# Performance work log

Hardware: AMD Instinct MI355X
Metric: run time of the kernel (lower is better)

## Reference

```python
import jax, jax.numpy as jnp
import numpy as np

B, C, H, WID = 32, 64, 128, 128
K = 5            # co-occurrence bins (co_shape)
WH = 3           # spatial filter height/width (w_shape = (1,3,3), depth 1)
ACT_LO, ACT_HI = 0.0, 1.0  # actBounds


def setup_inputs() -> dict:
    key = jax.random.key(0)
    k1, k2, k3 = jax.random.split(key, 3)
    input_tensor = jax.random.uniform(k1, (B, C, H, WID), dtype=jnp.float32)
    # learned params: L ~ N(0, 0.1) of shape (k,k); W ~ N(0,0.1) of shape (d,h,w)
    L = 0.1 * jax.random.normal(k2, (K, K), dtype=jnp.float32)
    W = 0.1 * jax.random.normal(k3, (1, WH, WH), dtype=jnp.float32)
    return {"input_tensor": input_tensor, "W": W, "L": L}


def _quantize(x, k):
    # map activation in [ACT_LO, ACT_HI] to bin index in [0, k-1]
    b = jnp.floor((x - ACT_LO) / (ACT_HI - ACT_LO) * k)
    return jnp.clip(b, 0, k - 1).astype(jnp.int32)


def reference(input_tensor, W, L):
    """Co-occurrence layer:
    out[p] = sum_{q in 3x3 nbhd(p)} W[q-p] * L[bin(x[q]), bin(x[p])] * x[q]
    Out-of-bounds neighbors contribute 0 (zero pad => x[q]=0 kills the term),
    matching the precomputed neighbor_lookup_table boundary handling.
    """
    k = L.shape[0]
    pad = WH // 2
    bins = _quantize(input_tensor, k)                      # (B,C,H,W) int32
    xp = jnp.pad(input_tensor, ((0, 0), (0, 0), (pad, pad), (pad, pad)))
    bp = jnp.pad(bins, ((0, 0), (0, 0), (pad, pad), (pad, pad)))
    h, w = input_tensor.shape[2], input_tensor.shape[3]
    out = jnp.zeros_like(input_tensor)
    for dh in range(WH):                                   # tiny fixed 3x3 loop
        for dw in range(WH):
            xn = xp[:, :, dh:dh + h, dw:dw + w]            # shifted neighbor values
            bn = bp[:, :, dh:dh + h, dw:dw + w]            # shifted neighbor bins
            out = out + W[0, dh, dw] * L[bn, bins] * xn    # gather L + weighted acc
    return out
```

## Files before the change

kernel.cpp:

```cpp
#include <hip/hip_runtime.h>


namespace {
constexpr int H  = 128;
constexpr int WD = 128;
constexpr int PLANES = 32 * 64;
constexpr int PX = 8;
constexpr int THREADS = 256;
}

__global__ __launch_bounds__(THREADS, 2) void col_kernel(
    const float* __restrict__ x, const float* __restrict__ Wf,
    const float* __restrict__ Lf, float* __restrict__ out)
{
    __shared__ float WL[9 * 25];
    const int t = threadIdx.x;
    if (t < 225) WL[t] = Wf[t / 25] * Lf[t % 25];
    __syncthreads();

    const int col0 = (t & 15) * PX;
    const int r0   = (t >> 4) * 8;

    const float* xp = x + (size_t)blockIdx.x * (H * WD);
    float* opb      = out + (size_t)blockIdx.x * (H * WD);
    const char* wlb = (const char*)WL;

    float win[4][PX + 2];
    int   bq[4][PX + 2];
    float n0[PX + 2], n1[PX + 2];

#define LOAD_ROW(DST, RR) {                                               \
    const int _rr = (RR);                                                 \
    if (_rr >= 0 && _rr < H) {                                            \
        const float* _rp = xp + _rr * WD + col0;                          \
        const float4 _c0 = *(const float4*)_rp;          \
        const float4 _c1 = *(const float4*)(_rp + 4);                     \
        DST[0] = (col0 > 0) ? _rp[-1] : 0.f;                              \
        DST[1] = _c0.x; DST[2] = _c0.y; DST[3] = _c0.z; DST[4] = _c0.w;   \
        DST[5] = _c1.x; DST[6] = _c1.y; DST[7] = _c1.z; DST[8] = _c1.w;   \
        DST[9] = (col0 < WD - PX) ? _rp[PX] : 0.f;                        \
    } else {                                                              \
        _Pragma("unroll")                                                 \
        for (int _j = 0; _j < PX + 2; ++_j) DST[_j] = 0.f;                \
    } }

#define QUANT_ROW(S) {                                                    \
    _Pragma("unroll")                                                     \
    for (int _j = 0; _j < PX + 2; ++_j) {                                 \
        int _b = (int)(win[S][_j] * 5.0f);        \
        _b = (_b > 4) ? 4 : _b;                                           \
        bq[S][_j] = _b * 20;                                              \
    } }

#define RETIRE(S, SRC) {                                                  \
    _Pragma("unroll")                                                     \
    for (int _j = 0; _j < PX + 2; ++_j) win[S][_j] = SRC[_j];             \
    QUANT_ROW(S) }

#define TERMS(QS, DR, BP, ACC) {                                          \
    _Pragma("unroll")                                                     \
    for (int _dw = 0; _dw < 3; ++_dw) {                                   \
        float _lw[PX];                                                    \
        _Pragma("unroll")                                                 \
        for (int _i = 0; _i < PX; ++_i)                                   \
            _lw[_i] = *(const float*)(wlb +                               \
                (bq[QS][_i + _dw] + BP[_i] + ((DR) * 3 + _dw) * 100));    \
        _Pragma("unroll")                                                 \
        for (int _i = 0; _i < PX; ++_i)                                   \
            ACC[_i] = fmaf(_lw[_i], win[QS][_i + _dw], ACC[_i]);          \
    } }

#define COMPUTE2(PA, PB, PC, PD, R) {                                     \
    int bp4a[PX], bp4b[PX];                                               \
    _Pragma("unroll")                                                     \
    for (int _i = 0; _i < PX; ++_i) {                                     \
        bp4a[_i] = (bq[PB][_i + 1] * 52429) >> 18;       \
        bp4b[_i] = (bq[PC][_i + 1] * 52429) >> 18;                        \
    }                                                                     \
    float acca[PX], accb[PX];                                             \
    _Pragma("unroll")                                                     \
    for (int _i = 0; _i < PX; ++_i) { acca[_i] = 0.f; accb[_i] = 0.f; }   \
    TERMS(PA, 0, bp4a, acca)                                              \
    TERMS(PB, 0, bp4b, accb)                                              \
    TERMS(PB, 1, bp4a, acca)                                              \
    TERMS(PC, 1, bp4b, accb)                                              \
    TERMS(PC, 2, bp4a, acca)                                              \
    TERMS(PD, 2, bp4b, accb)                                              \
    float* _op = opb + (R) * WD + col0;                                   \
    *(float4*)_op            = make_float4(acca[0], acca[1], acca[2], acca[3]); \
    *(float4*)(_op + 4)      = make_float4(acca[4], acca[5], acca[6], acca[7]); \
    *(float4*)(_op + WD)     = make_float4(accb[0], accb[1], accb[2], accb[3]); \
    *(float4*)(_op + WD + 4) = make_float4(accb[4], accb[5], accb[6], accb[7]); \
    }

    LOAD_ROW(win[0], r0 - 1) QUANT_ROW(0)
    LOAD_ROW(win[1], r0 + 0) QUANT_ROW(1)
    LOAD_ROW(win[2], r0 + 1) QUANT_ROW(2)
    LOAD_ROW(win[3], r0 + 2) QUANT_ROW(3)

    LOAD_ROW(n0, r0 + 3)
    LOAD_ROW(n1, r0 + 4)
    COMPUTE2(0, 1, 2, 3, r0)
    RETIRE(0, n0) RETIRE(1, n1)

    LOAD_ROW(n0, r0 + 5)
    LOAD_ROW(n1, r0 + 6)
    COMPUTE2(2, 3, 0, 1, r0 + 2)
    RETIRE(2, n0) RETIRE(3, n1)

    LOAD_ROW(n0, r0 + 7)
    LOAD_ROW(n1, r0 + 8)
    COMPUTE2(0, 1, 2, 3, r0 + 4)
    RETIRE(0, n0) RETIRE(1, n1)

    COMPUTE2(2, 3, 0, 1, r0 + 6)

#undef LOAD_ROW
#undef QUANT_ROW
#undef RETIRE
#undef TERMS
#undef COMPUTE2
}

extern "C" void kernel_launch(void* const* d_in, const int* in_sizes, int n_in,
                              void* d_out, int out_size, void* d_ws, size_t ws_size,
                              hipStream_t stream) {
    const float* x  = (const float*)d_in[0];
    const float* Wf = (const float*)d_in[1];
    const float* Lf = (const float*)d_in[2];
    float* out = (float*)d_out;

    col_kernel<<<dim3(PLANES), dim3(THREADS), 0, stream>>>(x, Wf, Lf, out);
}
```

Baseline: 252.2 us.

## Shrink register footprint with byte-packed bins and 3-row rolling window

Replaces the 4-row window plus two prefetch rows with a 3-row rolling window that computes one output row at a time, and packs the quantized bin offsets into bytes inside three ints per row. Launch bounds are raised from 2 to 5 blocks per CU to take advantage of the lower register use. The aim is higher occupancy to hide LDS-gather and global-load latency. In exchange there is less ILP per thread, less prefetch distance for the next row's loads, and extra shift/mask work to unpack each bin.

```diff
diff --git a/kernel.cpp b/kernel.cpp
--- a/kernel.cpp
+++ b/kernel.cpp
@@ -9,7 +9,7 @@
 constexpr int THREADS = 256;
 }
 
-__global__ __launch_bounds__(THREADS, 2) void col_kernel(
+__global__ __launch_bounds__(THREADS, 5) void col_kernel(
     const float* __restrict__ x, const float* __restrict__ Wf,
     const float* __restrict__ Lf, float* __restrict__ out)
 {
@@ -25,101 +25,87 @@
     float* opb      = out + (size_t)blockIdx.x * (H * WD);
     const char* wlb = (const char*)WL;
 
-    float win[4][PX + 2];
-    int   bq[4][PX + 2];
-    float n0[PX + 2], n1[PX + 2];
+    float win[3][PX + 2];
+    int   pk[3][3];
 
-#define LOAD_ROW(DST, RR) {                                               \
+#define LOAD_ROW(S, RR) {                                                 \
     const int _rr = (RR);                                                 \
     if (_rr >= 0 && _rr < H) {                                            \
         const float* _rp = xp + _rr * WD + col0;                          \
         const float4 _c0 = *(const float4*)_rp;          \
         const float4 _c1 = *(const float4*)(_rp + 4);                     \
-        DST[0] = (col0 > 0) ? _rp[-1] : 0.f;                              \
-        DST[1] = _c0.x; DST[2] = _c0.y; DST[3] = _c0.z; DST[4] = _c0.w;   \
-        DST[5] = _c1.x; DST[6] = _c1.y; DST[7] = _c1.z; DST[8] = _c1.w;   \
-        DST[9] = (col0 < WD - PX) ? _rp[PX] : 0.f;                        \
+        win[S][0] = (col0 > 0) ? _rp[-1] : 0.f;                           \
+        win[S][1] = _c0.x; win[S][2] = _c0.y;                             \
+        win[S][3] = _c0.z; win[S][4] = _c0.w;                             \
+        win[S][5] = _c1.x; win[S][6] = _c1.y;                             \
+        win[S][7] = _c1.z; win[S][8] = _c1.w;                             \
+        win[S][9] = (col0 < WD - PX) ? _rp[PX] : 0.f;                     \
     } else {                                                              \
         _Pragma("unroll")                                                 \
-        for (int _j = 0; _j < PX + 2; ++_j) DST[_j] = 0.f;                \
+        for (int _j = 0; _j < PX + 2; ++_j) win[S][_j] = 0.f;             \
     } }
 
-#define QUANT_ROW(S) {                                                    \
+#define QPACK(S) {                                                        \
+    int _b[PX + 2];                                                       \
     _Pragma("unroll")                                                     \
     for (int _j = 0; _j < PX + 2; ++_j) {                                 \
-        int _b = (int)(win[S][_j] * 5.0f);        \
-        _b = (_b > 4) ? 4 : _b;                                           \
-        bq[S][_j] = _b * 20;                                              \
-    } }
+        int _v = (int)(win[S][_j] * 5.0f);        \
+        _v = (_v > 4) ? 4 : _v;                                           \
+        _b[_j] = _v * 20;                                                 \
+    }                                                                     \
+    pk[S][0] = _b[0] | (_b[1] << 8) | (_b[2] << 16) | (_b[3] << 24);      \
+    pk[S][1] = _b[4] | (_b[5] << 8) | (_b[6] << 16) | (_b[7] << 24);      \
+    pk[S][2] = _b[8] | (_b[9] << 8); }
 
-#define RETIRE(S, SRC) {                                                  \
-    _Pragma("unroll")                                                     \
-    for (int _j = 0; _j < PX + 2; ++_j) win[S][_j] = SRC[_j];             \
-    QUANT_ROW(S) }
+#define BF(S, J) ((pk[S][(J) >> 2] >> (8 * ((J) & 3))) & 0xff)
 
-#define TERMS(QS, DR, BP, ACC) {                                          \
+#define TERMS(QS, DR) {                                                   \
     _Pragma("unroll")                                                     \
     for (int _dw = 0; _dw < 3; ++_dw) {                                   \
         float _lw[PX];                                                    \
         _Pragma("unroll")                                                 \
         for (int _i = 0; _i < PX; ++_i)                                   \
             _lw[_i] = *(const float*)(wlb +                               \
-                (bq[QS][_i + _dw] + BP[_i] + ((DR) * 3 + _dw) * 100));    \
+                (BF(QS, _i + _dw) + bp4[_i] + ((DR) * 3 + _dw) * 100));   \
         _Pragma("unroll")                                                 \
         for (int _i = 0; _i < PX; ++_i)                                   \
-            ACC[_i] = fmaf(_lw[_i], win[QS][_i + _dw], ACC[_i]);          \
+            acc[_i] = fmaf(_lw[_i], win[QS][_i + _dw], acc[_i]);          \
     } }
 
-#define COMPUTE2(PA, PB, PC, PD, R) {                                     \
-    int bp4a[PX], bp4b[PX];                                               \
+#define COMPUTE(A, B, C, R) {                                             \
+    int bp4[PX];                                                          \
     _Pragma("unroll")                                                     \
-    for (int _i = 0; _i < PX; ++_i) {                                     \
-        bp4a[_i] = (bq[PB][_i + 1] * 52429) >> 18;       \
-        bp4b[_i] = (bq[PC][_i + 1] * 52429) >> 18;                        \
-    }                                                                     \
-    float acca[PX], accb[PX];                                             \
+    for (int _i = 0; _i < PX; ++_i)                                       \
+        bp4[_i] = (BF(B, _i + 1) * 52429) >> 18;         \
+    float acc[PX];                                                        \
     _Pragma("unroll")                                                     \
-    for (int _i = 0; _i < PX; ++_i) { acca[_i] = 0.f; accb[_i] = 0.f; }   \
-    TERMS(PA, 0, bp4a, acca)                                              \
-    TERMS(PB, 0, bp4b, accb)                                              \
-    TERMS(PB, 1, bp4a, acca)                                              \
-    TERMS(PC, 1, bp4b, accb)                                              \
-    TERMS(PC, 2, bp4a, acca)                                              \
-    TERMS(PD, 2, bp4b, accb)                                              \
+    for (int _i = 0; _i < PX; ++_i) acc[_i] = 0.f;                        \
+    TERMS(A, 0)                                                           \
+    TERMS(B, 1)                                                           \
+    TERMS(C, 2)                                                           \
     float* _op = opb + (R) * WD + col0;                                   \
-    *(float4*)_op            = make_float4(acca[0], acca[1], acca[2], acca[3]); \
-    *(float4*)(_op + 4)      = make_float4(acca[4], acca[5], acca[6], acca[7]); \
-    *(float4*)(_op + WD)     = make_float4(accb[0], accb[1], accb[2], accb[3]); \
-    *(float4*)(_op + WD + 4) = make_float4(accb[4], accb[5], accb[6], accb[7]); \
+    *(float4*)_op       = make_float4(acc[0], acc[1], acc[2], acc[3]);    \
+    *(float4*)(_op + 4) = make_float4(acc[4], acc[5], acc[6], acc[7]);    \
     }
 
-    LOAD_ROW(win[0], r0 - 1) QUANT_ROW(0)
-    LOAD_ROW(win[1], r0 + 0) QUANT_ROW(1)
-    LOAD_ROW(win[2], r0 + 1) QUANT_ROW(2)
-    LOAD_ROW(win[3], r0 + 2) QUANT_ROW(3)
+    LOAD_ROW(0, r0 - 1) QPACK(0)
+    LOAD_ROW(1, r0 + 0) QPACK(1)
+    LOAD_ROW(2, r0 + 1) QPACK(2)
 
-    LOAD_ROW(n0, r0 + 3)
-    LOAD_ROW(n1, r0 + 4)
-    COMPUTE2(0, 1, 2, 3, r0)
-    RETIRE(0, n0) RETIRE(1, n1)
-
-    LOAD_ROW(n0, r0 + 5)
-    LOAD_ROW(n1, r0 + 6)
-    COMPUTE2(2, 3, 0, 1, r0 + 2)
-    RETIRE(2, n0) RETIRE(3, n1)
-
-    LOAD_ROW(n0, r0 + 7)
-    LOAD_ROW(n1, r0 + 8)
-    COMPUTE2(0, 1, 2, 3, r0 + 4)
-    RETIRE(0, n0) RETIRE(1, n1)
-
-    COMPUTE2(2, 3, 0, 1, r0 + 6)
+    COMPUTE(0, 1, 2, r0 + 0)  LOAD_ROW(0, r0 + 2) QPACK(0)
+    COMPUTE(1, 2, 0, r0 + 1)  LOAD_ROW(1, r0 + 3) QPACK(1)
+    COMPUTE(2, 0, 1, r0 + 2)  LOAD_ROW(2, r0 + 4) QPACK(2)
+    COMPUTE(0, 1, 2, r0 + 3)  LOAD_ROW(0, r0 + 5) QPACK(0)
+    COMPUTE(1, 2, 0, r0 + 4)  LOAD_ROW(1, r0 + 6) QPACK(1)
+    COMPUTE(2, 0, 1, r0 + 5)  LOAD_ROW(2, r0 + 7) QPACK(2)
+    COMPUTE(0, 1, 2, r0 + 6)  LOAD_ROW(0, r0 + 8) QPACK(0)
+    COMPUTE(1, 2, 0, r0 + 7)
 
 #undef LOAD_ROW
-#undef QUANT_ROW
-#undef RETIRE
+#undef QPACK
+#undef BF
 #undef TERMS
-#undef COMPUTE2
+#undef COMPUTE
 }
 
 extern "C" void kernel_launch(void* const* d_in, const int* in_sizes, int n_in,
```

Measured after the change: 253.7 us. No clear change (+0.6%).
